# Optimization experiments

Hardware: AMD Instinct MI355X
Metric: run time of the kernel (lower is better)

The kernel has to match this reference:

```python
import jax, jax.numpy as jnp
import numpy as np

C = 64
B, H, W = 2, 128, 512
SCALE = C ** (-0.5)


def conv1x1(x, w, b):
    # x: [B,C,H,W], w: [O,I], b: [O]
    return jnp.einsum('bihw,oi->bohw', x, w) + b[None, :, None, None]


def dwconv3x3(x, w, b):
    # depthwise 3x3, w: [C,1,3,3]
    y = jax.lax.conv_general_dilated(
        x, w, window_strides=(1, 1), padding='SAME',
        feature_group_count=x.shape[1],
        dimension_numbers=('NCHW', 'OIHW', 'NCHW'))
    return y + b[None, :, None, None]


def proj12(x, w1, b1, wd, bd):
    return dwconv3x3(conv1x1(x, w1, b1), wd, bd)


def setup_inputs() -> dict:
    key = jax.random.key(0)
    ks = jax.random.split(key, 32)
    d = {}
    d['x_l'] = jax.random.normal(ks[0], (B, C, H, W), dtype=jnp.float32)
    d['x_r'] = jax.random.normal(ks[1], (B, C, H, W), dtype=jnp.float32)
    i = 2
    for p in ['lp1', 'rp1', 'lp2', 'rp2']:
        d[p + '_w1'] = jax.random.normal(ks[i], (C, C), dtype=jnp.float32) * 0.05; i += 1
        d[p + '_b1'] = jnp.zeros((C,), dtype=jnp.float32)
        d[p + '_wd'] = jax.random.normal(ks[i], (C, 1, 3, 3), dtype=jnp.float32) * 0.1; i += 1
        d[p + '_bd'] = jnp.zeros((C,), dtype=jnp.float32)
    for p in ['lp3', 'rp3']:
        d[p + '_w'] = jax.random.normal(ks[i], (C, C), dtype=jnp.float32) * 0.05; i += 1
        d[p + '_b'] = jnp.zeros((C,), dtype=jnp.float32)
    return d


def reference(x_l, x_r,
              lp1_w1, lp1_b1, lp1_wd, lp1_bd,
              rp1_w1, rp1_b1, rp1_wd, rp1_bd,
              lp2_w1, lp2_b1, lp2_wd, lp2_bd,
              rp2_w1, rp2_b1, rp2_wd, rp2_bd,
              lp3_w, lp3_b, rp3_w, rp3_b):
    Ql = proj12(x_l, lp1_w1, lp1_b1, lp1_wd, lp1_bd)  # [B,C,H,W]
    Qr = proj12(x_r, rp1_w1, rp1_b1, rp1_wd, rp1_bd)  # [B,C,H,W]
    # attention[b,h,w,v] = sum_c Ql[b,c,h,w] * Qr[b,c,h,v]
    att = jnp.einsum('bchw,bchv->bhwv', Ql, Qr) * SCALE  # [B,H,W,W]
    Vl = proj12(x_l, lp2_w1, lp2_b1, lp2_wd, lp2_bd)
    Vr = proj12(x_r, rp2_w1, rp2_b1, rp2_wd, rp2_bd)
    # softmax over right-view width (last axis), aggregate Vr
    A_r2l = jax.nn.softmax(att, axis=-1)
    F_r2l = jnp.einsum('bhwv,bchv->bchw', A_r2l, Vr)  # [B,C,H,W]
    # transposed attention, softmax over left-view width (axis -2 of att)
    A_l2r = jax.nn.softmax(att, axis=-2)
    F_l2r = jnp.einsum('bhwv,bchw->bchv', A_l2r, Vl)  # [B,C,H,W]
    F_r2l = conv1x1(F_r2l, lp3_w, lp3_b)
    F_l2r = conv1x1(F_l2r, rp3_w, rp3_b)
    return x_l + F_r2l + x_r + F_l2r
```

## Files before the change

### kernel.cpp

```cpp
#include <hip/hip_runtime.h>
#include <hip/hip_bf16.h>

typedef __attribute__((ext_vector_type(8))) short short8;
typedef __attribute__((ext_vector_type(4))) float f32x4;

#define QSCALE 0.18033688011112042f

__device__ __forceinline__ unsigned short f2bf(float f){
    unsigned u = __float_as_uint(f);
    unsigned r = (u + 0x7fffu + ((u>>16)&1u))>>16;
    return (unsigned short)r;
}
__device__ __forceinline__ unsigned pk_rtne(float hi, float lo){
    return (((unsigned)f2bf(hi))<<16) | (unsigned)f2bf(lo);
}

__global__ __launch_bounds__(256) void init_out_k(const float* __restrict__ xl,
                                                  const float* __restrict__ xr,
                                                  float* __restrict__ out, int n4){
    int i = blockIdx.x*256 + threadIdx.x;
    if (i < n4){
        const float4* a = (const float4*)xl;
        const float4* b = (const float4*)xr;
        float4 va = a[i], vb = b[i];
        float4 vo; vo.x=va.x+vb.x; vo.y=va.y+vb.y; vo.z=va.z+vb.z; vo.w=va.w+vb.w;
        ((float4*)out)[i] = vo;
    }
}

__global__ __launch_bounds__(256) void gemm_k(const float* __restrict__ x,
                                              const float* __restrict__ w1,
                                              const float* __restrict__ b1,
                                              unsigned short* __restrict__ T){
    __shared__ __align__(16) short sA[256*72];
    __shared__ __align__(16) short sB[64*72];
    __shared__ float sbias[64];
    int tid = threadIdx.x;
    int b = blockIdx.x >> 8;
    int hw0 = (blockIdx.x & 255) << 8;
    {
        int c = tid & 63, pq = tid >> 6;
        const float* xb = x + ((size_t)b<<22) + (size_t)c*65536 + hw0;
        #pragma unroll
        for (int it=0; it<16; it++){
            int piece = pq*16 + it;
            float4 v = *(const float4*)(xb + piece*4);
            int p = piece*4;
            sA[(p+0)*72 + c] = (short)f2bf(v.x);
            sA[(p+1)*72 + c] = (short)f2bf(v.y);
            sA[(p+2)*72 + c] = (short)f2bf(v.z);
            sA[(p+3)*72 + c] = (short)f2bf(v.w);
        }
        #pragma unroll
        for (int it=0; it<16; it++){
            int lin = it*256 + tid;
            int o = lin >> 6, cc = lin & 63;
            sB[o*72 + cc] = (short)f2bf(w1[lin]);
        }
        if (tid < 64) sbias[tid] = b1[tid];
    }
    __syncthreads();
    int wv = tid>>6, lane = tid&63, quad = lane>>4, l16 = lane&15;
    int m0 = wv*64;
    short8 a0[4], a1[4], bB0[4], bB1[4];
    #pragma unroll
    for (int mt=0; mt<4; mt++){
        a0[mt] = *(const short8*)(sA + (m0 + mt*16 + l16)*72 + quad*8);
        a1[mt] = *(const short8*)(sA + (m0 + mt*16 + l16)*72 + 32 + quad*8);
    }
    #pragma unroll
    for (int nt=0; nt<4; nt++){
        bB0[nt] = *(const short8*)(sB + (nt*16 + l16)*72 + quad*8);
        bB1[nt] = *(const short8*)(sB + (nt*16 + l16)*72 + 32 + quad*8);
    }
    const f32x4 z4 = {0.f,0.f,0.f,0.f};
    f32x4 acc[4][4];
    #pragma unroll
    for (int mt=0; mt<4; mt++)
        #pragma unroll
        for (int nt=0; nt<4; nt++){
            acc[mt][nt] = __builtin_amdgcn_mfma_f32_16x16x32_bf16(a0[mt], bB0[nt], z4, 0,0,0);
            acc[mt][nt] = __builtin_amdgcn_mfma_f32_16x16x32_bf16(a1[mt], bB1[nt], acc[mt][nt], 0,0,0);
        }
    int px0 = blockIdx.x << 8;
    #pragma unroll
    for (int nt=0; nt<4; nt++){
        float bias = sbias[nt*16 + l16];
        #pragma unroll
        for (int mt=0; mt<4; mt++){
            #pragma unroll
            for (int r=0;r<4;r++){
                int pxr = px0 + m0 + mt*16 + quad*4 + r;
                T[(size_t)pxr*64 + nt*16 + l16] = f2bf(acc[mt][nt][r] + bias);
            }
        }
    }
}

__global__ __launch_bounds__(256) void dwconv_k(const unsigned short* __restrict__ T,
                                                const float* __restrict__ wd,
                                                const float* __restrict__ bd,
                                                unsigned short* __restrict__ dst,
                                                int modeQ, float qscale){
    int bid = blockIdx.x;
    int wt = bid & 7, h = (bid>>3)&127, b = bid>>10;
    int tid = threadIdx.x;
    int cg = tid & 15, wl = tid >> 4;
    int c0 = cg*4;
    int w0 = wt*64 + wl*4;
    float acc[4][4];
    #pragma unroll
    for (int ch=0; ch<4; ch++){
        float bv = bd[c0+ch];
        #pragma unroll
        for (int i=0;i<4;i++) acc[ch][i] = bv;
    }
    const unsigned short* Tb = T + ((size_t)b<<22);
    #pragma unroll
    for (int dh=-1; dh<=1; dh++){
        int hh = h + dh;
        if (hh < 0 || hh > 127) continue;
        const unsigned short* Tr = Tb + ((size_t)(hh*512))*64 + c0;
        float win[6][4];
        #pragma unroll
        for (int j=0;j<6;j++){
            int ww = w0 - 1 + j;
            if (ww >= 0 && ww < 512){
                uint2 v = *(const uint2*)(Tr + (size_t)ww*64);
                win[j][0] = __uint_as_float(v.x<<16);
                win[j][1] = __uint_as_float(v.x & 0xffff0000u);
                win[j][2] = __uint_as_float(v.y<<16);
                win[j][3] = __uint_as_float(v.y & 0xffff0000u);
            } else {
                win[j][0]=0.f; win[j][1]=0.f; win[j][2]=0.f; win[j][3]=0.f;
            }
        }
        #pragma unroll
        for (int ch=0; ch<4; ch++){
            float k0 = wd[(c0+ch)*9 + (dh+1)*3];
            float k1 = wd[(c0+ch)*9 + (dh+1)*3 + 1];
            float k2 = wd[(c0+ch)*9 + (dh+1)*3 + 2];
            #pragma unroll
            for (int i=0;i<4;i++)
                acc[ch][i] += k0*win[i][ch] + k1*win[i+1][ch] + k2*win[i+2][ch];
        }
    }
    if (modeQ){
        int base = (b*128 + h)*512;
        #pragma unroll
        for (int i=0;i<4;i++){
            uint2 v;
            v.x = pk_rtne(acc[1][i]*qscale, acc[0][i]*qscale);
            v.y = pk_rtne(acc[3][i]*qscale, acc[2][i]*qscale);
            *(uint2*)(dst + ((size_t)(base + w0 + i))*64 + c0) = v;
        }
    } else {
        #pragma unroll
        for (int ch=0; ch<4; ch++){
            uint2 v;
            v.x = pk_rtne(acc[ch][1], acc[ch][0]);
            v.y = pk_rtne(acc[ch][3], acc[ch][2]);
            *(uint2*)(dst + (((size_t)(b*64 + c0 + ch))<<16) + h*512 + w0) = v;
        }
    }
}

#define PQ 72
#define PK 72
#define PV 72
#define PP 72
#define PW 72
#define PFA 72
#define POT 17
#define OFF_Q   0
#define OFF_K   9216
#define OFF_V   18432
#define OFF_W3  27648
#define LDS_TOT 36864

__global__ __launch_bounds__(256) void flash_k(
    const unsigned short* __restrict__ Ql, const unsigned short* __restrict__ Qr,
    const unsigned short* __restrict__ Vl, const unsigned short* __restrict__ Vr,
    const float* __restrict__ lw3, const float* __restrict__ lb3,
    const float* __restrict__ rw3, const float* __restrict__ rb3,
    float* __restrict__ out)
{
    __shared__ __align__(16) char smem[LDS_TOT];
    short* sQ  = (short*)(smem + OFF_Q);
    short* sK  = (short*)(smem + OFF_K);
    short* sV  = (short*)(smem + OFF_V);
    short* sP  = (short*)(smem + OFF_Q);
    short* sW  = (short*)(smem + OFF_W3);
    short* sFA = (short*)(smem + OFF_Q);
    float* sOT = (float*)(smem + OFF_K);

    int bid = blockIdx.x;
    int g  = ((bid >> 6) << 3) | (bid & 7);
    int qt = (bid >> 3) & 7;
    int h = g & 127, b = (g >> 7) & 1, dir = g >> 8;
    const unsigned short *Qg, *Kg, *Vg; const float *w3, *b3;
    if (dir==0){ Qg = Ql; Kg = Qr; Vg = Vr; w3 = lw3; b3 = lb3; }
    else       { Qg = Qr; Kg = Ql; Vg = Vl; w3 = rw3; b3 = rb3; }

    int tid = threadIdx.x;
    int wv = tid>>6, lane = tid&63, quad = lane>>4, l16 = lane&15;
    int bh = b*128 + h;

    {
        const uint4* src = (const uint4*)(Qg + ((size_t)bh*512 + qt*64)*64);
        #pragma unroll
        for (int it=0; it<2; it++){
            int idx = it*256 + tid;
            int row = idx>>3, piece = idx&7;
            *(uint4*)(sQ + row*PQ + piece*8) = src[idx];
        }
        #pragma unroll
        for (int it=0; it<16; it++){
            int idx = it*256 + tid;
            int o = idx>>6, cc = idx&63;
            sW[o*PW + cc] = (short)f2bf(w3[idx]);
        }
    }
    __syncthreads();

    short8 aq0 = *(const short8*)(sQ + (wv*16 + l16)*PQ + quad*8);
    short8 aq1 = *(const short8*)(sQ + (wv*16 + l16)*PQ + 32 + quad*8);

    const f32x4 z4 = {0.f,0.f,0.f,0.f};
    f32x4 oacc[4];
    #pragma unroll
    for (int ct=0; ct<4; ct++) oacc[ct] = z4;
    float lps = 0.f;

    const uint4* Ksrc = (const uint4*)(Kg + (size_t)bh*512*64);
    const unsigned short* Vbase = Vg + ((size_t)(b*64)*128 + h)*512;
    short* sPw = sP + wv*16*PP;

    for (int kt=0; kt<8; kt++){
        #pragma unroll
        for (int it=0; it<2; it++){
            int idx = it*256 + tid;
            int row = idx>>3, piece = idx&7;
            *(uint4*)(sK + row*PK + piece*8) = Ksrc[(size_t)(kt*64 + row)*8 + piece];
            uint4 vv = *(const uint4*)(Vbase + (size_t)row*65536 + kt*64 + piece*8);
            *(uint4*)(sV + row*PV + piece*8) = vv;
        }
        __syncthreads();
        #pragma unroll
        for (int nt=0; nt<4; nt++){
            short8 bk0 = *(const short8*)(sK + (nt*16 + l16)*PK + quad*8);
            short8 bk1 = *(const short8*)(sK + (nt*16 + l16)*PK + 32 + quad*8);
            f32x4 s = __builtin_amdgcn_mfma_f32_16x16x32_bf16(bk0, aq0, z4, 0,0,0);
            s       = __builtin_amdgcn_mfma_f32_16x16x32_bf16(bk1, aq1, s, 0,0,0);
            float p0 = __builtin_amdgcn_exp2f(s[0]);
            float p1 = __builtin_amdgcn_exp2f(s[1]);
            float p2 = __builtin_amdgcn_exp2f(s[2]);
            float p3 = __builtin_amdgcn_exp2f(s[3]);
            lps += (p0+p1) + (p2+p3);
            unsigned lo = __builtin_amdgcn_perm(__float_as_uint(p1), __float_as_uint(p0), 0x07060302);
            unsigned hi = __builtin_amdgcn_perm(__float_as_uint(p3), __float_as_uint(p2), 0x07060302);
            uint2 pv; pv.x = lo; pv.y = hi;
            *(uint2*)(sPw + l16*PP + nt*16 + quad*4) = pv;
        }
        short8 ap0 = *(const short8*)(sPw + l16*PP + quad*8);
        short8 ap1 = *(const short8*)(sPw + l16*PP + 32 + quad*8);
        #pragma unroll
        for (int ct=0; ct<4; ct++){
            short8 bv0 = *(const short8*)(sV + (ct*16 + l16)*PV + quad*8);
            short8 bv1 = *(const short8*)(sV + (ct*16 + l16)*PV + 32 + quad*8);
            oacc[ct] = __builtin_amdgcn_mfma_f32_16x16x32_bf16(ap0, bv0, oacc[ct], 0,0,0);
            oacc[ct] = __builtin_amdgcn_mfma_f32_16x16x32_bf16(ap1, bv1, oacc[ct], 0,0,0);
        }
        __syncthreads();
    }

    float l = lps;
    l += __shfl_xor(l, 16);
    l += __shfl_xor(l, 32);
    float inv[4];
    #pragma unroll
    for (int r=0;r<4;r++) inv[r] = 1.0f / __shfl(l, quad*4 + r);

    short* sFw = sFA + wv*16*PFA;
    #pragma unroll
    for (int ct=0; ct<4; ct++){
        #pragma unroll
        for (int r=0;r<4;r++)
            sFw[(quad*4+r)*PFA + ct*16 + l16] = (short)f2bf(oacc[ct][r]*inv[r]);
    }
    short8 af0 = *(const short8*)(sFw + l16*PFA + quad*8);
    short8 af1 = *(const short8*)(sFw + l16*PFA + 32 + quad*8);
    f32x4 d2[4];
    #pragma unroll
    for (int ot=0; ot<4; ot++){
        short8 bw0 = *(const short8*)(sW + (ot*16 + l16)*PW + quad*8);
        short8 bw1 = *(const short8*)(sW + (ot*16 + l16)*PW + 32 + quad*8);
        d2[ot] = __builtin_amdgcn_mfma_f32_16x16x32_bf16(af0, bw0, z4, 0,0,0);
        d2[ot] = __builtin_amdgcn_mfma_f32_16x16x32_bf16(af1, bw1, d2[ot], 0,0,0);
        float bias = b3[ot*16 + l16];
        #pragma unroll
        for (int r=0;r<4;r++) d2[ot][r] += bias;
    }
    __syncthreads();
    float* sOw = sOT + wv*(64*POT);
    #pragma unroll
    for (int ot=0; ot<4; ot++){
        #pragma unroll
        for (int r=0;r<4;r++)
            sOw[(ot*16 + l16)*POT + quad*4 + r] = d2[ot][r];
    }
    int wbase = qt*64 + wv*16;
    #pragma unroll
    for (int it=0; it<16; it++){
        int o = it*4 + quad;
        float val = sOw[o*POT + l16];
        unsafeAtomicAdd(out + ((size_t)(b*64 + o)*128 + h)*512 + wbase + l16, val);
    }
}

extern "C" void kernel_launch(void* const* d_in, const int* in_sizes, int n_in,
                              void* d_out, int out_size, void* d_ws, size_t ws_size,
                              hipStream_t stream)
{
    const float* xl = (const float*)d_in[0];
    const float* xr = (const float*)d_in[1];
    const float* lp1_w1 = (const float*)d_in[2];
    const float* lp1_b1 = (const float*)d_in[3];
    const float* lp1_wd = (const float*)d_in[4];
    const float* lp1_bd = (const float*)d_in[5];
    const float* rp1_w1 = (const float*)d_in[6];
    const float* rp1_b1 = (const float*)d_in[7];
    const float* rp1_wd = (const float*)d_in[8];
    const float* rp1_bd = (const float*)d_in[9];
    const float* lp2_w1 = (const float*)d_in[10];
    const float* lp2_b1 = (const float*)d_in[11];
    const float* lp2_wd = (const float*)d_in[12];
    const float* lp2_bd = (const float*)d_in[13];
    const float* rp2_w1 = (const float*)d_in[14];
    const float* rp2_b1 = (const float*)d_in[15];
    const float* rp2_wd = (const float*)d_in[16];
    const float* rp2_bd = (const float*)d_in[17];
    const float* lp3_w  = (const float*)d_in[18];
    const float* lp3_b  = (const float*)d_in[19];
    const float* rp3_w  = (const float*)d_in[20];
    const float* rp3_b  = (const float*)d_in[21];
    float* out = (float*)d_out;

    const size_t S = 16777216;
    char* ws = (char*)d_ws;
    unsigned short* T   = (unsigned short*)(ws);
    unsigned short* Ql  = (unsigned short*)(ws + 1*S);
    unsigned short* Qr  = (unsigned short*)(ws + 2*S);
    unsigned short* Vl  = (unsigned short*)(ws + 3*S);
    unsigned short* Vr  = (unsigned short*)(ws + 4*S);

    init_out_k<<<8192, 256, 0, stream>>>(xl, xr, out, 2097152);

    gemm_k<<<512, 256, 0, stream>>>(xl, lp1_w1, lp1_b1, T);
    dwconv_k<<<2048, 256, 0, stream>>>(T, lp1_wd, lp1_bd, Ql, 1, QSCALE);
    gemm_k<<<512, 256, 0, stream>>>(xl, lp2_w1, lp2_b1, T);
    dwconv_k<<<2048, 256, 0, stream>>>(T, lp2_wd, lp2_bd, Vl, 0, 1.0f);

    gemm_k<<<512, 256, 0, stream>>>(xr, rp1_w1, rp1_b1, T);
    dwconv_k<<<2048, 256, 0, stream>>>(T, rp1_wd, rp1_bd, Qr, 1, 1.0f);
    gemm_k<<<512, 256, 0, stream>>>(xr, rp2_w1, rp2_b1, T);
    dwconv_k<<<2048, 256, 0, stream>>>(T, rp2_wd, rp2_bd, Vr, 0, 1.0f);

    flash_k<<<4096, 256, 0, stream>>>(Ql, Qr, Vl, Vr, lp3_w, lp3_b, rp3_w, rp3_b, out);
}
```

Before: 340.1 us.

## Fuse Q/V projections per view, double flash query tile, prefetch K/V

```diff
diff --git a/kernel.cpp b/kernel.cpp
--- a/kernel.cpp
+++ b/kernel.cpp
@@ -29,12 +29,15 @@
 }
 
 __global__ __launch_bounds__(256) void gemm_k(const float* __restrict__ x,
-                                              const float* __restrict__ w1,
-                                              const float* __restrict__ b1,
-                                              unsigned short* __restrict__ T){
+                                              const float* __restrict__ wA,
+                                              const float* __restrict__ bA,
+                                              const float* __restrict__ wB,
+                                              const float* __restrict__ bB,
+                                              unsigned short* __restrict__ T1,
+                                              unsigned short* __restrict__ T2){
     __shared__ __align__(16) short sA[256*72];
-    __shared__ __align__(16) short sB[64*72];
-    __shared__ float sbias[64];
+    __shared__ __align__(16) short sB[128*72];
+    __shared__ float sbias[128];
     int tid = threadIdx.x;
     int b = blockIdx.x >> 8;
     int hw0 = (blockIdx.x & 255) << 8;
@@ -52,70 +55,67 @@
             sA[(p+3)*72 + c] = (short)f2bf(v.w);
         }
         #pragma unroll
-        for (int it=0; it<16; it++){
+        for (int it=0; it<32; it++){
             int lin = it*256 + tid;
             int o = lin >> 6, cc = lin & 63;
-            sB[o*72 + cc] = (short)f2bf(w1[lin]);
-        }
-        if (tid < 64) sbias[tid] = b1[tid];
+            float wv = (o < 64) ? wA[o*64 + cc] : wB[(o-64)*64 + cc];
+            sB[o*72 + cc] = (short)f2bf(wv);
+        }
+        if (tid < 128) sbias[tid] = (tid < 64) ? bA[tid] : bB[tid-64];
     }
     __syncthreads();
     int wv = tid>>6, lane = tid&63, quad = lane>>4, l16 = lane&15;
     int m0 = wv*64;
-    short8 a0[4], a1[4], bB0[4], bB1[4];
+    short8 a0[4], a1[4];
     #pragma unroll
     for (int mt=0; mt<4; mt++){
         a0[mt] = *(const short8*)(sA + (m0 + mt*16 + l16)*72 + quad*8);
         a1[mt] = *(const short8*)(sA + (m0 + mt*16 + l16)*72 + 32 + quad*8);
     }
-    #pragma unroll
-    for (int nt=0; nt<4; nt++){
-        bB0[nt] = *(const short8*)(sB + (nt*16 + l16)*72 + quad*8);
-        bB1[nt] = *(const short8*)(sB + (nt*16 + l16)*72 + 32 + quad*8);
-    }
     const f32x4 z4 = {0.f,0.f,0.f,0.f};
-    f32x4 acc[4][4];
-    #pragma unroll
-    for (int mt=0; mt<4; mt++)
+    int px0 = blockIdx.x << 8;
+    #pragma unroll
+    for (int set=0; set<2; set++){
+        unsigned short* T = set ? T2 : T1;
+        short8 bB0[4], bB1[4];
         #pragma unroll
         for (int nt=0; nt<4; nt++){
-            acc[mt][nt] = __builtin_amdgcn_mfma_f32_16x16x32_bf16(a0[mt], bB0[nt], z4, 0,0,0);
-            acc[mt][nt] = __builtin_amdgcn_mfma_f32_16x16x32_bf16(a1[mt], bB1[nt], acc[mt][nt], 0,0,0);
-        }
-    int px0 = blockIdx.x << 8;
-    #pragma unroll
-    for (int nt=0; nt<4; nt++){
-        float bias = sbias[nt*16 + l16];
-        #pragma unroll
-        for (int mt=0; mt<4; mt++){
-            #pragma unroll
-            for (int r=0;r<4;r++){
-                int pxr = px0 + m0 + mt*16 + quad*4 + r;
-                T[(size_t)pxr*64 + nt*16 + l16] = f2bf(acc[mt][nt][r] + bias);
-            }
-        }
-    }
-}
-
-__global__ __launch_bounds__(256) void dwconv_k(const unsigned short* __restrict__ T,
-                                                const float* __restrict__ wd,
-                                                const float* __restrict__ bd,
-                                                unsigned short* __restrict__ dst,
-                                                int modeQ, float qscale){
-    int bid = blockIdx.x;
-    int wt = bid & 7, h = (bid>>3)&127, b = bid>>10;
-    int tid = threadIdx.x;
-    int cg = tid & 15, wl = tid >> 4;
-    int c0 = cg*4;
-    int w0 = wt*64 + wl*4;
-    float acc[4][4];
+            bB0[nt] = *(const short8*)(sB + (set*64 + nt*16 + l16)*72 + quad*8);
+            bB1[nt] = *(const short8*)(sB + (set*64 + nt*16 + l16)*72 + 32 + quad*8);
+        }
+        f32x4 acc[4][4];
+        #pragma unroll
+        for (int mt=0; mt<4; mt++)
+            #pragma unroll
+            for (int nt=0; nt<4; nt++){
+                acc[mt][nt] = __builtin_amdgcn_mfma_f32_16x16x32_bf16(a0[mt], bB0[nt], z4, 0,0,0);
+                acc[mt][nt] = __builtin_amdgcn_mfma_f32_16x16x32_bf16(a1[mt], bB1[nt], acc[mt][nt], 0,0,0);
+            }
+        #pragma unroll
+        for (int nt=0; nt<4; nt++){
+            float bias = sbias[set*64 + nt*16 + l16];
+            #pragma unroll
+            for (int mt=0; mt<4; mt++){
+                #pragma unroll
+                for (int r=0;r<4;r++){
+                    int pxr = px0 + m0 + mt*16 + quad*4 + r;
+                    T[(size_t)pxr*64 + nt*16 + l16] = f2bf(acc[mt][nt][r] + bias);
+                }
+            }
+        }
+    }
+}
+
+__device__ __forceinline__ void dw_tile(const unsigned short* __restrict__ Tb,
+                                        const float* __restrict__ wd,
+                                        const float* __restrict__ bd,
+                                        int c0, int w0, int h, float acc[4][4]){
     #pragma unroll
     for (int ch=0; ch<4; ch++){
         float bv = bd[c0+ch];
         #pragma unroll
         for (int i=0;i<4;i++) acc[ch][i] = bv;
     }
-    const unsigned short* Tb = T + ((size_t)b<<22);
     #pragma unroll
     for (int dh=-1; dh<=1; dh++){
         int hh = h + dh;
@@ -145,22 +145,43 @@
                 acc[ch][i] += k0*win[i][ch] + k1*win[i+1][ch] + k2*win[i+2][ch];
         }
     }
-    if (modeQ){
+}
+
+__global__ __launch_bounds__(256) void dwconv_k(const unsigned short* __restrict__ T1,
+                                                const unsigned short* __restrict__ T2,
+                                                const float* __restrict__ wd1,
+                                                const float* __restrict__ bd1,
+                                                const float* __restrict__ wd2,
+                                                const float* __restrict__ bd2,
+                                                unsigned short* __restrict__ Qdst,
+                                                unsigned short* __restrict__ Vdst,
+                                                float qscale){
+    int bid = blockIdx.x;
+    int wt = bid & 7, h = (bid>>3)&127, b = bid>>10;
+    int tid = threadIdx.x;
+    int cg = tid & 15, wl = tid >> 4;
+    int c0 = cg*4;
+    int w0 = wt*64 + wl*4;
+    float acc[4][4];
+    dw_tile(T1 + ((size_t)b<<22), wd1, bd1, c0, w0, h, acc);
+    {
         int base = (b*128 + h)*512;
         #pragma unroll
         for (int i=0;i<4;i++){
             uint2 v;
             v.x = pk_rtne(acc[1][i]*qscale, acc[0][i]*qscale);
             v.y = pk_rtne(acc[3][i]*qscale, acc[2][i]*qscale);
-            *(uint2*)(dst + ((size_t)(base + w0 + i))*64 + c0) = v;
-        }
-    } else {
+            *(uint2*)(Qdst + ((size_t)(base + w0 + i))*64 + c0) = v;
+        }
+    }
+    dw_tile(T2 + ((size_t)b<<22), wd2, bd2, c0, w0, h, acc);
+    {
         #pragma unroll
         for (int ch=0; ch<4; ch++){
             uint2 v;
             v.x = pk_rtne(acc[ch][1], acc[ch][0]);
             v.y = pk_rtne(acc[ch][3], acc[ch][2]);
-            *(uint2*)(dst + (((size_t)(b*64 + c0 + ch))<<16) + h*512 + w0) = v;
+            *(uint2*)(Vdst + (((size_t)(b*64 + c0 + ch))<<16) + h*512 + w0) = v;
         }
     }
 }
@@ -169,16 +190,14 @@
 #define PK 72
 #define PV 72
 #define PP 72
-#define PW 72
 #define PFA 72
 #define POT 17
 #define OFF_Q   0
-#define OFF_K   9216
-#define OFF_V   18432
-#define OFF_W3  27648
+#define OFF_K   18432
+#define OFF_V   27648
 #define LDS_TOT 36864
 
-__global__ __launch_bounds__(256) void flash_k(
+__global__ __launch_bounds__(256,4) void flash_k(
     const unsigned short* __restrict__ Ql, const unsigned short* __restrict__ Qr,
     const unsigned short* __restrict__ Vl, const unsigned short* __restrict__ Vr,
     const float* __restrict__ lw3, const float* __restrict__ lb3,
@@ -190,13 +209,12 @@
     short* sK  = (short*)(smem + OFF_K);
     short* sV  = (short*)(smem + OFF_V);
     short* sP  = (short*)(smem + OFF_Q);
-    short* sW  = (short*)(smem + OFF_W3);
     short* sFA = (short*)(smem + OFF_Q);
     float* sOT = (float*)(smem + OFF_K);
 
     int bid = blockIdx.x;
-    int g  = ((bid >> 6) << 3) | (bid & 7);
-    int qt = (bid >> 3) & 7;
+    int g  = ((bid >> 5) << 3) | (bid & 7);
+    int qt = (bid >> 3) & 3;
     int h = g & 127, b = (g >> 7) & 1, dir = g >> 8;
     const unsigned short *Qg, *Kg, *Vg; const float *w3, *b3;
     if (dir==0){ Qg = Ql; Kg = Qr; Vg = Vr; w3 = lw3; b3 = lb3; }
@@ -207,114 +225,163 @@
     int bh = b*128 + h;
 
     {
-        const uint4* src = (const uint4*)(Qg + ((size_t)bh*512 + qt*64)*64);
+        const uint4* src = (const uint4*)(Qg + ((size_t)bh*512 + qt*128)*64);
+        #pragma unroll
+        for (int it=0; it<4; it++){
+            int idx = it*256 + tid;
+            int row = idx>>3, piece = idx&7;
+            *(uint4*)(sQ + row*PQ + piece*8) = src[idx];
+        }
+    }
+    __syncthreads();
+
+    short8 aq0[2], aq1[2];
+    #pragma unroll
+    for (int s=0; s<2; s++){
+        aq0[s] = *(const short8*)(sQ + (wv*32 + s*16 + l16)*PQ + quad*8);
+        aq1[s] = *(const short8*)(sQ + (wv*32 + s*16 + l16)*PQ + 32 + quad*8);
+    }
+
+    const f32x4 z4 = {0.f,0.f,0.f,0.f};
+    f32x4 oacc[2][4];
+    #pragma unroll
+    for (int s=0; s<2; s++)
+        #pragma unroll
+        for (int ct=0; ct<4; ct++) oacc[s][ct] = z4;
+    float lps[2] = {0.f, 0.f};
+
+    const uint4* Ksrc = (const uint4*)(Kg + (size_t)bh*512*64);
+    const unsigned short* Vbase = Vg + ((size_t)(b*64)*128 + h)*512;
+
+    uint4 kreg[2], vreg[2];
+    #pragma unroll
+    for (int it=0; it<2; it++){
+        int idx = it*256 + tid;
+        int row = idx>>3, piece = idx&7;
+        kreg[it] = Ksrc[(size_t)row*8 + piece];
+        vreg[it] = *(const uint4*)(Vbase + (size_t)row*65536 + piece*8);
+    }
+
+    for (int kt=0; kt<8; kt++){
         #pragma unroll
         for (int it=0; it<2; it++){
             int idx = it*256 + tid;
             int row = idx>>3, piece = idx&7;
-            *(uint4*)(sQ + row*PQ + piece*8) = src[idx];
-        }
-        #pragma unroll
-        for (int it=0; it<16; it++){
-            int idx = it*256 + tid;
-            int o = idx>>6, cc = idx&63;
-            sW[o*PW + cc] = (short)f2bf(w3[idx]);
-        }
-    }
-    __syncthreads();
-
-    short8 aq0 = *(const short8*)(sQ + (wv*16 + l16)*PQ + quad*8);
-    short8 aq1 = *(const short8*)(sQ + (wv*16 + l16)*PQ + 32 + quad*8);
-
-    const f32x4 z4 = {0.f,0.f,0.f,0.f};
-    f32x4 oacc[4];
-    #pragma unroll
-    for (int ct=0; ct<4; ct++) oacc[ct] = z4;
-    float lps = 0.f;
-
-    const uint4* Ksrc = (const uint4*)(Kg + (size_t)bh*512*64);
-    const unsigned short* Vbase = Vg + ((size_t)(b*64)*128 + h)*512;
-    short* sPw = sP + wv*16*PP;
-
-    for (int kt=0; kt<8; kt++){
-        #pragma unroll
-        for (int it=0; it<2; it++){
-            int idx = it*256 + tid;
-            int row = idx>>3, piece = idx&7;
-            *(uint4*)(sK + row*PK + piece*8) = Ksrc[(size_t)(kt*64 + row)*8 + piece];
-            uint4 vv = *(const uint4*)(Vbase + (size_t)row*65536 + kt*64 + piece*8);
-            *(uint4*)(sV + row*PV + piece*8) = vv;
+            *(uint4*)(sK + row*PK + piece*8) = kreg[it];
+            *(uint4*)(sV + row*PV + piece*8) = vreg[it];
         }
         __syncthreads();
+        if (kt < 7){
+            #pragma unroll
+            for (int it=0; it<2; it++){
+                int idx = it*256 + tid;
+                int row = idx>>3, piece = idx&7;
+                kreg[it] = Ksrc[(size_t)((kt+1)*64 + row)*8 + piece];
+                vreg[it] = *(const uint4*)(Vbase + (size_t)row*65536 + (kt+1)*64 + piece*8);
+            }
+        }
         #pragma unroll
         for (int nt=0; nt<4; nt++){
             short8 bk0 = *(const short8*)(sK + (nt*16 + l16)*PK + quad*8);
             short8 bk1 = *(const short8*)(sK + (nt*16 + l16)*PK + 32 + quad*8);
-            f32x4 s = __builtin_amdgcn_mfma_f32_16x16x32_bf16(bk0, aq0, z4, 0,0,0);
-            s       = __builtin_amdgcn_mfma_f32_16x16x32_bf16(bk1, aq1, s, 0,0,0);
-            float p0 = __builtin_amdgcn_exp2f(s[0]);
-            float p1 = __builtin_amdgcn_exp2f(s[1]);
-            float p2 = __builtin_amdgcn_exp2f(s[2]);
-            float p3 = __builtin_amdgcn_exp2f(s[3]);
-            lps += (p0+p1) + (p2+p3);
-            unsigned lo = __builtin_amdgcn_perm(__float_as_uint(p1), __float_as_uint(p0), 0x07060302);
-            unsigned hi = __builtin_amdgcn_perm(__float_as_uint(p3), __float_as_uint(p2), 0x07060302);
-            uint2 pv; pv.x = lo; pv.y = hi;
-            *(uint2*)(sPw + l16*PP + nt*16 + quad*4) = pv;
-        }
-        short8 ap0 = *(const short8*)(sPw + l16*PP + quad*8);
-        short8 ap1 = *(const short8*)(sPw + l16*PP + 32 + quad*8);
+            #pragma unroll
+            for (int s=0; s<2; s++){
+                f32x4 sv = __builtin_amdgcn_mfma_f32_16x16x32_bf16(bk0, aq0[s], z4, 0,0,0);
+                sv       = __builtin_amdgcn_mfma_f32_16x16x32_bf16(bk1, aq1[s], sv, 0,0,0);
+                float p0 = __builtin_amdgcn_exp2f(sv[0]);
+                float p1 = __builtin_amdgcn_exp2f(sv[1]);
+                float p2 = __builtin_amdgcn_exp2f(sv[2]);
+                float p3 = __builtin_amdgcn_exp2f(sv[3]);
+                lps[s] += (p0+p1) + (p2+p3);
+                unsigned lo = __builtin_amdgcn_perm(__float_as_uint(p1), __float_as_uint(p0), 0x07060302);
+                unsigned hi = __builtin_amdgcn_perm(__float_as_uint(p3), __float_as_uint(p2), 0x07060302);
+                uint2 pv; pv.x = lo; pv.y = hi;
+                *(uint2*)(sP + (wv*32 + s*16 + l16)*PP + nt*16 + quad*4) = pv;
+            }
+        }
+        short8 ap0[2], ap1[2];
+        #pragma unroll
+        for (int s=0; s<2; s++){
+            ap0[s] = *(const short8*)(sP + (wv*32 + s*16 + l16)*PP + quad*8);
+            ap1[s] = *(const short8*)(sP + (wv*32 + s*16 + l16)*PP + 32 + quad*8);
+        }
         #pragma unroll
         for (int ct=0; ct<4; ct++){
             short8 bv0 = *(const short8*)(sV + (ct*16 + l16)*PV + quad*8);
             short8 bv1 = *(const short8*)(sV + (ct*16 + l16)*PV + 32 + quad*8);
-            oacc[ct] = __builtin_amdgcn_mfma_f32_16x16x32_bf16(ap0, bv0, oacc[ct], 0,0,0);
-            oacc[ct] = __builtin_amdgcn_mfma_f32_16x16x32_bf16(ap1, bv1, oacc[ct], 0,0,0);
+            #pragma unroll
+            for (int s=0; s<2; s++){
+                oacc[s][ct] = __builtin_amdgcn_mfma_f32_16x16x32_bf16(ap0[s], bv0, oacc[s][ct], 0,0,0);
+                oacc[s][ct] = __builtin_amdgcn_mfma_f32_16x16x32_bf16(ap1[s], bv1, oacc[s][ct], 0,0,0);
+            }
         }
         __syncthreads();
     }
 
-    float l = lps;
-    l += __shfl_xor(l, 16);
-    l += __shfl_xor(l, 32);
-    float inv[4];
-    #pragma unroll
-    for (int r=0;r<4;r++) inv[r] = 1.0f / __shfl(l, quad*4 + r);
-
-    short* sFw = sFA + wv*16*PFA;
-    #pragma unroll
-    for (int ct=0; ct<4; ct++){
-        #pragma unroll
-        for (int r=0;r<4;r++)
-            sFw[(quad*4+r)*PFA + ct*16 + l16] = (short)f2bf(oacc[ct][r]*inv[r]);
-    }
-    short8 af0 = *(const short8*)(sFw + l16*PFA + quad*8);
-    short8 af1 = *(const short8*)(sFw + l16*PFA + 32 + quad*8);
-    f32x4 d2[4];
+    float inv[2][4];
+    #pragma unroll
+    for (int s=0; s<2; s++){
+        float l = lps[s];
+        l += __shfl_xor(l, 16);
+        l += __shfl_xor(l, 32);
+        #pragma unroll
+        for (int r=0;r<4;r++) inv[s][r] = 1.0f / __shfl(l, quad*4 + r);
+    }
+
+    #pragma unroll
+    for (int s=0; s<2; s++){
+        short* sFw = sFA + (wv*32 + s*16)*PFA;
+        #pragma unroll
+        for (int ct=0; ct<4; ct++){
+            #pragma unroll
+            for (int r=0;r<4;r++)
+                sFw[(quad*4+r)*PFA + ct*16 + l16] = (short)f2bf(oacc[s][ct][r]*inv[s][r]);
+        }
+    }
+    short8 af0[2], af1[2];
+    #pragma unroll
+    for (int s=0; s<2; s++){
+        af0[s] = *(const short8*)(sFA + (wv*32 + s*16 + l16)*PFA + quad*8);
+        af1[s] = *(const short8*)(sFA + (wv*32 + s*16 + l16)*PFA + 32 + quad*8);
+    }
+    f32x4 d2[2][4];
     #pragma unroll
     for (int ot=0; ot<4; ot++){
-        short8 bw0 = *(const short8*)(sW + (ot*16 + l16)*PW + quad*8);
-        short8 bw1 = *(const short8*)(sW + (ot*16 + l16)*PW + 32 + quad*8);
-        d2[ot] = __builtin_amdgcn_mfma_f32_16x16x32_bf16(af0, bw0, z4, 0,0,0);
-        d2[ot] = __builtin_amdgcn_mfma_f32_16x16x32_bf16(af1, bw1, d2[ot], 0,0,0);
+        const float* wrow = w3 + (ot*16 + l16)*64 + quad*8;
+        float4 wa = *(const float4*)(wrow);
+        float4 wb = *(const float4*)(wrow + 4);
+        float4 wc = *(const float4*)(wrow + 32);
+        float4 wd = *(const float4*)(wrow + 36);
+        short8 bw0, bw1;
+        bw0[0]=(short)f2bf(wa.x); bw0[1]=(short)f2bf(wa.y); bw0[2]=(short)f2bf(wa.z); bw0[3]=(short)f2bf(wa.w);
+        bw0[4]=(short)f2bf(wb.x); bw0[5]=(short)f2bf(wb.y); bw0[6]=(short)f2bf(wb.z); bw0[7]=(short)f2bf(wb.w);
+        bw1[0]=(short)f2bf(wc.x); bw1[1]=(short)f2bf(wc.y); bw1[2]=(short)f2bf(wc.z); bw1[3]=(short)f2bf(wc.w);
+        bw1[4]=(short)f2bf(wd.x); bw1[5]=(short)f2bf(wd.y); bw1[6]=(short)f2bf(wd.z); bw1[7]=(short)f2bf(wd.w);
         float bias = b3[ot*16 + l16];
         #pragma unroll
-        for (int r=0;r<4;r++) d2[ot][r] += bias;
-    }
-    __syncthreads();
+        for (int s=0; s<2; s++){
+            d2[s][ot] = __builtin_amdgcn_mfma_f32_16x16x32_bf16(af0[s], bw0, z4, 0,0,0);
+            d2[s][ot] = __builtin_amdgcn_mfma_f32_16x16x32_bf16(af1[s], bw1, d2[s][ot], 0,0,0);
+            #pragma unroll
+            for (int r=0;r<4;r++) d2[s][ot][r] += bias;
+        }
+    }
     float* sOw = sOT + wv*(64*POT);
     #pragma unroll
-    for (int ot=0; ot<4; ot++){
-        #pragma unroll
-        for (int r=0;r<4;r++)
-            sOw[(ot*16 + l16)*POT + quad*4 + r] = d2[ot][r];
-    }
-    int wbase = qt*64 + wv*16;
-    #pragma unroll
-    for (int it=0; it<16; it++){
-        int o = it*4 + quad;
-        float val = sOw[o*POT + l16];
-        unsafeAtomicAdd(out + ((size_t)(b*64 + o)*128 + h)*512 + wbase + l16, val);
+    for (int s=0; s<2; s++){
+        #pragma unroll
+        for (int ot=0; ot<4; ot++){
+            #pragma unroll
+            for (int r=0;r<4;r++)
+                sOw[(ot*16 + l16)*POT + quad*4 + r] = d2[s][ot][r];
+        }
+        int qbase = qt*128 + wv*32 + s*16;
+        #pragma unroll
+        for (int it=0; it<16; it++){
+            int o = it*4 + quad;
+            float val = sOw[o*POT + l16];
+            unsafeAtomicAdd(out + ((size_t)(b*64 + o)*128 + h)*512 + qbase + l16, val);
+        }
     }
 }
 
@@ -348,23 +415,20 @@
 
     const size_t S = 16777216;
     char* ws = (char*)d_ws;
-    unsigned short* T   = (unsigned short*)(ws);
-    unsigned short* Ql  = (unsigned short*)(ws + 1*S);
-    unsigned short* Qr  = (unsigned short*)(ws + 2*S);
-    unsigned short* Vl  = (unsigned short*)(ws + 3*S);
-    unsigned short* Vr  = (unsigned short*)(ws + 4*S);
+    unsigned short* T1  = (unsigned short*)(ws);
+    unsigned short* T2  = (unsigned short*)(ws + 1*S);
+    unsigned short* Ql  = (unsigned short*)(ws + 2*S);
+    unsigned short* Qr  = (unsigned short*)(ws + 3*S);
+    unsigned short* Vl  = (unsigned short*)(ws + 4*S);
+    unsigned short* Vr  = (unsigned short*)(ws + 5*S);
 
     init_out_k<<<8192, 256, 0, stream>>>(xl, xr, out, 2097152);
 
-    gemm_k<<<512, 256, 0, stream>>>(xl, lp1_w1, lp1_b1, T);
-    dwconv_k<<<2048, 256, 0, stream>>>(T, lp1_wd, lp1_bd, Ql, 1, QSCALE);
-    gemm_k<<<512, 256, 0, stream>>>(xl, lp2_w1, lp2_b1, T);
-    dwconv_k<<<2048, 256, 0, stream>>>(T, lp2_wd, lp2_bd, Vl, 0, 1.0f);
-
-    gemm_k<<<512, 256, 0, stream>>>(xr, rp1_w1, rp1_b1, T);
-    dwconv_k<<<2048, 256, 0, stream>>>(T, rp1_wd, rp1_bd, Qr, 1, 1.0f);
-    gemm_k<<<512, 256, 0, stream>>>(xr, rp2_w1, rp2_b1, T);
-    dwconv_k<<<2048, 256, 0, stream>>>(T, rp2_wd, rp2_bd, Vr, 0, 1.0f);
-
-    flash_k<<<4096, 256, 0, stream>>>(Ql, Qr, Vl, Vr, lp3_w, lp3_b, rp3_w, rp3_b, out);
-}
+    gemm_k<<<512, 256, 0, stream>>>(xl, lp1_w1, lp1_b1, lp2_w1, lp2_b1, T1, T2);
+    dwconv_k<<<2048, 256, 0, stream>>>(T1, T2, lp1_wd, lp1_bd, lp2_wd, lp2_bd, Ql, Vl, QSCALE);
+
+    gemm_k<<<512, 256, 0, stream>>>(xr, rp1_w1, rp1_b1, rp2_w1, rp2_b1, T1, T2);
+    dwconv_k<<<2048, 256, 0, stream>>>(T1, T2, rp1_wd, rp1_bd, rp2_wd, rp2_bd, Qr, Vr, 1.0f);
+
+    flash_k<<<2048, 256, 0, stream>>>(Ql, Qr, Vl, Vr, lp3_w, lp3_b, rp3_w, rp3_b, out);
+}
```

New measurement: 363.8 us. +6.9%, slower.
